# Kernel optimization log

Hardware: AMD Instinct MI355X
Metric: run time of the kernel (lower is better)

Reference implementation:

```python
import jax, jax.numpy as jnp
import numpy as np

N_NODES = 50000
NUM_FEATURES = 128
HIDDEN = 128
OUT = 64
N_EDGES = 600000


def gcn_conv(x, edge_index, W, b, n_nodes):
    """PyG GCNConv: add self-loops, symmetric deg^{-1/2} normalization,
    x' = D^{-1/2}(A+I)D^{-1/2} (x @ W) + b."""
    xw = x @ W  # [N, out]
    loop = jnp.arange(n_nodes, dtype=edge_index.dtype)
    row = jnp.concatenate([edge_index[0], loop])  # source
    col = jnp.concatenate([edge_index[1], loop])  # target
    ones = jnp.ones(row.shape[0], dtype=xw.dtype)
    deg = jax.ops.segment_sum(ones, col, num_segments=n_nodes)  # in-degree incl. self-loop
    dis = jnp.where(deg > 0, jax.lax.rsqrt(deg), 0.0)
    norm = dis[row] * dis[col]  # [E+N]
    msg = xw[row] * norm[:, None]  # gather + scale
    agg = jax.ops.segment_sum(msg, col, num_segments=n_nodes)  # scatter-add
    return agg + b


def setup_inputs() -> dict:
    key = jax.random.key(0)
    ks = jax.random.split(key, 10)
    x = jax.random.normal(ks[0], (N_NODES, NUM_FEATURES), dtype=jnp.float32)
    edge_index = jax.random.randint(ks[1], (2, N_EDGES), 0, N_NODES, dtype=jnp.int64)
    s1 = 1.0 / np.sqrt(NUM_FEATURES)
    s2 = 1.0 / np.sqrt(HIDDEN)
    s3 = 1.0 / np.sqrt(OUT)
    # encoder GCN weights stored as [in, out]
    W_enc1 = jax.random.uniform(ks[2], (NUM_FEATURES, HIDDEN), jnp.float32, -s1, s1)
    b_enc1 = jnp.zeros((HIDDEN,), jnp.float32)
    W_enc2 = jax.random.uniform(ks[3], (HIDDEN, OUT), jnp.float32, -s2, s2)
    b_enc2 = jnp.zeros((OUT,), jnp.float32)
    # decoder Linear weights stored as [in, out]
    W_dec1 = jax.random.uniform(ks[4], (OUT, HIDDEN), jnp.float32, -s3, s3)
    b_dec1 = jax.random.uniform(ks[5], (HIDDEN,), jnp.float32, -s3, s3)
    W_dec2 = jax.random.uniform(ks[6], (HIDDEN, NUM_FEATURES), jnp.float32, -s2, s2)
    b_dec2 = jax.random.uniform(ks[7], (NUM_FEATURES,), jnp.float32, -s2, s2)
    return {"x": x, "edge_index": edge_index,
            "W_enc1": W_enc1, "b_enc1": b_enc1,
            "W_enc2": W_enc2, "b_enc2": b_enc2,
            "W_dec1": W_dec1, "b_dec1": b_dec1,
            "W_dec2": W_dec2, "b_dec2": b_dec2}


def reference(x, edge_index, W_enc1, b_enc1, W_enc2, b_enc2,
              W_dec1, b_dec1, W_dec2, b_dec2):
    n = x.shape[0]
    z = jax.nn.relu(gcn_conv(x, edge_index, W_enc1, b_enc1, n))
    z = jax.nn.relu(gcn_conv(z, edge_index, W_enc2, b_enc2, n))
    z = jax.nn.relu(z @ W_dec1 + b_dec1)
    x_hat = z @ W_dec2 + b_dec2
    return x_hat
```

## Files before the change

kernel.cpp:

```cpp
#include <hip/hip_runtime.h>
#include <hip/hip_bf16.h>


#define N_FEAT 128
#define HID    128
#define OUTD   64

typedef __hip_bfloat16 bf16;
typedef unsigned short u16;
typedef __attribute__((ext_vector_type(8))) short short8;
typedef __attribute__((ext_vector_type(4))) float f32x4;

__device__ __forceinline__ float bs2f(short s) {
    return __builtin_bit_cast(float, ((unsigned)(unsigned short)s) << 16);
}
__device__ __forceinline__ short f2bs(float f) {
    __hip_bfloat16 h = __float2bfloat16(f);
    return __builtin_bit_cast(short, h);
}


__global__ void k_prep(int* __restrict__ cnt, int n, int ZB,
                       const float* __restrict__ W1, const float* __restrict__ W2,
                       const float* __restrict__ Wd1, const float* __restrict__ Wd2,
                       bf16* __restrict__ W1t, bf16* __restrict__ W2t,
                       bf16* __restrict__ Wd1t, bf16* __restrict__ Wd2t) {
    int b = blockIdx.x;
    if (b < ZB) {
        int i4 = b * 256 + threadIdx.x;
        int n4 = n >> 2;
        if (i4 < n4) ((int4*)cnt)[i4] = make_int4(0, 0, 0, 0);
        if (i4 == 0) for (int i = n4 * 4; i < n; ++i) cnt[i] = 0;
        return;
    }
    int i = (b - ZB) * 256 + threadIdx.x;
    if (i < 16384) {
        int k = i >> 7, nn = i & 127;
        W1t[nn * 128 + k] = __float2bfloat16(W1[i]);
    } else if (i < 24576) {
        int j = i - 16384; int k = j >> 6, nn = j & 63;
        W2t[nn * 128 + k] = __float2bfloat16(W2[j]);
    } else if (i < 32768) {
        int j = i - 24576; int k = j >> 7, nn = j & 127;
        Wd1t[nn * 64 + k] = __float2bfloat16(Wd1[j]);
    } else if (i < 49152) {
        int j = i - 32768; int k = j >> 7, nn = j & 127;
        Wd2t[nn * 128 + k] = __float2bfloat16(Wd2[j]);
    }
}


__global__ void k_mega(const int* __restrict__ row, const int* __restrict__ col,
                       int E, int SL, int npg, int GB,
                       int* __restrict__ cnt, u16* __restrict__ slots, int n,
                       const float* __restrict__ x, const bf16* __restrict__ W1t,
                       bf16* __restrict__ xw1) {
    int b = blockIdx.x;
    if (b < GB) {
        if (b * 64 >= n) return;
        int t = threadIdx.x;
        int lane = t & 63, w = t >> 6;
        int quad = lane >> 4, l16 = lane & 15;
        int m0 = b * 64 + (w & 1) * 32;
        int nhw = (w >> 1) * 32;
        int kq = quad * 8;

        short8 zero8 = {0, 0, 0, 0, 0, 0, 0, 0};
        int mrow[2]; bool mok[2];
#pragma unroll
        for (int mi = 0; mi < 2; ++mi) {
            mrow[mi] = m0 + mi * 16 + l16;
            mok[mi] = mrow[mi] < n;
        }
        short8 af[2][4];
#pragma unroll
        for (int mi = 0; mi < 2; ++mi) {
#pragma unroll
            for (int kb = 0; kb < 4; ++kb) {
                if (!mok[mi]) { af[mi][kb] = zero8; continue; }
                const float* Af = x + (size_t)mrow[mi] * 128 + kb * 32 + kq;
                float4 a4 = *(const float4*)Af;
                float4 b4 = *(const float4*)(Af + 4);
                short8 r = {f2bs(a4.x), f2bs(a4.y), f2bs(a4.z), f2bs(a4.w),
                            f2bs(b4.x), f2bs(b4.y), f2bs(b4.z), f2bs(b4.w)};
                af[mi][kb] = r;
            }
        }
#pragma unroll
        for (int nc = 0; nc < 128; nc += 64) {
            int n0 = nc + nhw;
            f32x4 acc[2][2];
#pragma unroll
            for (int mi = 0; mi < 2; ++mi)
#pragma unroll
                for (int ni = 0; ni < 2; ++ni)
#pragma unroll
                    for (int r = 0; r < 4; ++r) acc[mi][ni][r] = 0.f;
#pragma unroll
            for (int kb = 0; kb < 4; ++kb) {
                short8 bfm[2];
#pragma unroll
                for (int ni = 0; ni < 2; ++ni) {
                    int nn = n0 + ni * 16 + l16;
                    bfm[ni] = *(const short8*)(W1t + (size_t)nn * 128 + kb * 32 + kq);
                }
#pragma unroll
                for (int mi = 0; mi < 2; ++mi)
#pragma unroll
                    for (int ni = 0; ni < 2; ++ni)
                        acc[mi][ni] = __builtin_amdgcn_mfma_f32_16x16x32_bf16(
                            af[mi][kb], bfm[ni], acc[mi][ni], 0, 0, 0);
            }
#pragma unroll
            for (int ni = 0; ni < 2; ++ni) {
                int nn = n0 + ni * 16 + l16;
#pragma unroll
                for (int mi = 0; mi < 2; ++mi)
#pragma unroll
                    for (int r = 0; r < 4; ++r) {
                        int m = m0 + mi * 16 + quad * 4 + r;
                        if (m < n)
                            ((short*)xw1)[(size_t)m * 128 + nn] = f2bs(acc[mi][ni][r]);
                    }
            }
        }
        return;
    }
    int bb = b - GB;
    int g = bb & 7;
    int s = bb >> 3;
    int lo = g * npg;
    int hi = lo + npg; if (hi > n) hi = n;
    int i4 = s * 256 + threadIdx.x;
    int E4 = E >> 2;
    if (i4 < E4) {
        int4 r4 = ((const int4*)row)[i4];
        int4 c4 = ((const int4*)col)[i4];
        int rr[4] = {r4.x, r4.y, r4.z, r4.w};
        int cc[4] = {c4.x, c4.y, c4.z, c4.w};
#pragma unroll
        for (int u = 0; u < 4; ++u) {
            int r = rr[u], c = cc[u];
            if (c >= lo && c < hi && (unsigned)r < (unsigned)n) {
                int pos = atomicAdd(&cnt[c], 1);
                if (pos < 64) slots[(size_t)c * 64 + pos] = (u16)r;
            }
        }
    }
    if (i4 == 0) {
        for (int e = E4 * 4; e < E; ++e) {
            int r = row[e], c = col[e];
            if (c >= lo && c < hi && (unsigned)r < (unsigned)n) {
                int pos = atomicAdd(&cnt[c], 1);
                if (pos < 64) slots[(size_t)c * 64 + pos] = (u16)r;
            }
        }
    }
}


__global__ void k_aggmm(const bf16* __restrict__ xw1, const int* __restrict__ cnt,
                        const u16* __restrict__ slots, const float* __restrict__ b1,
                        const bf16* __restrict__ W2t, bf16* __restrict__ xw2, int M) {
    __shared__ short h1s[64][136];
    __shared__ u16 sl_s[64][72];
    __shared__ float dn_s[64];
    __shared__ int cn_s[64];
    int t = threadIdx.x;
    int lane = t & 63, w = t >> 6;
    int blk = blockIdx.x;

    if (t < 64) {
        int nd = blk * 64 + t;
        int craw = (nd < M) ? cnt[nd] : -1;
        cn_s[t] = (nd < M) ? (min(craw, 64) + 1) : 0;
        dn_s[t] = (nd < M) ? rsqrtf((float)(craw + 1)) : 0.f;
    }
    {
        int node = t >> 3, chunk = t & 7;
        int nd = blk * 64 + node;
        int4 val = make_int4(0, 0, 0, 0);
        if (nd < M)
            val = ((const int4*)(slots + (size_t)nd * 64))[chunk];
        *(int4*)&sl_s[node][chunk * 8] = val;
    }
    __syncthreads();

    int sub = lane >> 4, li = lane & 15;
    float4 c0 = *(const float4*)(b1 + li * 8);
    float4 c1 = *(const float4*)(b1 + li * 8 + 4);
    float bbv[8] = {c0.x, c0.y, c0.z, c0.w, c1.x, c1.y, c1.z, c1.w};

#pragma unroll
    for (int rnd = 0; rnd < 2; ++rnd) {
        int nl = w * 8 + rnd * 4 + sub;
        int nd = blk * 64 + nl;
        int cn = cn_s[nl];
        float a[8] = {0.f, 0.f, 0.f, 0.f, 0.f, 0.f, 0.f, 0.f};
        for (int tt = 0; tt < cn; tt += 8) {
            bool va[8]; short8 v[8]; float dsv[8];
#pragma unroll
            for (int u = 0; u < 8; ++u) {
                int ti = tt + u;
                va[u] = ti < cn;
                int tc = va[u] ? ti : 0;
                int sI = (tc == cn - 1) ? nd : (int)sl_s[nl][tc];
                v[u] = *((const short8*)(xw1 + (size_t)sI * 128) + li);
                dsv[u] = rsqrtf((float)(cnt[sI] + 1));
            }
#pragma unroll
            for (int u = 0; u < 8; ++u)
                if (va[u]) {
#pragma unroll
                    for (int j = 0; j < 8; ++j) a[j] += dsv[u] * bs2f(v[u][j]);
                }
        }
        float dn = dn_s[nl];
        short8 o;
#pragma unroll
        for (int j = 0; j < 8; ++j) o[j] = f2bs(fmaxf(dn * a[j] + bbv[j], 0.f));
        *(short8*)&h1s[nl][li * 8] = o;
    }
    __syncthreads();

    int quad = lane >> 4, l16 = lane & 15;
    int mt = w & 3;
    int nh = w >> 2;
    int kq = quad * 8;

    short8 af[4];
#pragma unroll
    for (int kb = 0; kb < 4; ++kb)
        af[kb] = *(const short8*)&h1s[mt * 16 + l16][kb * 32 + kq];

    f32x4 acc[2];
#pragma unroll
    for (int ni = 0; ni < 2; ++ni)
#pragma unroll
        for (int r = 0; r < 4; ++r) acc[ni][r] = 0.f;
#pragma unroll
    for (int kb = 0; kb < 4; ++kb) {
        short8 bfm[2];
#pragma unroll
        for (int ni = 0; ni < 2; ++ni) {
            int nn = nh * 32 + ni * 16 + l16;
            bfm[ni] = *(const short8*)(W2t + (size_t)nn * 128 + kb * 32 + kq);
        }
#pragma unroll
        for (int ni = 0; ni < 2; ++ni)
            acc[ni] = __builtin_amdgcn_mfma_f32_16x16x32_bf16(
                af[kb], bfm[ni], acc[ni], 0, 0, 0);
    }
#pragma unroll
    for (int ni = 0; ni < 2; ++ni) {
        int nn = nh * 32 + ni * 16 + l16;
#pragma unroll
        for (int r = 0; r < 4; ++r) {
            int ml = mt * 16 + quad * 4 + r;
            int m = blk * 64 + ml;
            if (m < M)
                ((short*)xw2)[(size_t)m * 64 + nn] = f2bs(acc[ni][r] * dn_s[ml]);
        }
    }
}


__global__ void k_aggdec(const bf16* __restrict__ xw2, const int* __restrict__ cnt,
                         const u16* __restrict__ slots,
                         const float* __restrict__ b2,
                         const bf16* __restrict__ Wd1t, const float* __restrict__ bd1,
                         const bf16* __restrict__ Wd2t, const float* __restrict__ bd2,
                         float* __restrict__ out, int M) {
    __shared__ short h2s[64][72];
    __shared__ short h3s[64][136];
    int t = threadIdx.x;
    int lane = t & 63, w = t >> 6;
    int quad = lane >> 4, l16 = lane & 15;
    int blk = blockIdx.x;

    {
        int sub = lane >> 3;
        int li = lane & 7;
        int sgl = w * 8 + sub;
        int nd0 = blk * 64 + sgl;
        int nd1 = nd0 + 32;
        int cr0 = (nd0 < M) ? cnt[nd0] : -1;
        int cr1 = (nd1 < M) ? cnt[nd1] : -1;
        int cn0 = (nd0 < M) ? min(cr0, 64) + 1 : 0;
        int cn1 = (nd1 < M) ? min(cr1, 64) + 1 : 0;
        const u16* sl0 = slots + (size_t)min(nd0, M - 1) * 64;
        const u16* sl1 = slots + (size_t)min(nd1, M - 1) * 64;

        float a0[8] = {0.f, 0.f, 0.f, 0.f, 0.f, 0.f, 0.f, 0.f};
        float a1[8] = {0.f, 0.f, 0.f, 0.f, 0.f, 0.f, 0.f, 0.f};
        int tmax = cn0 > cn1 ? cn0 : cn1;
        for (int e = 0; e < tmax; e += 4) {
            bool va0[4], va1[4]; short8 v0[4], v1[4];
#pragma unroll
            for (int u = 0; u < 4; ++u) {
                int ei_ = e + u;
                va0[u] = ei_ < cn0;
                int t0 = va0[u] ? ei_ : 0;
                int s0 = (t0 == cn0 - 1) ? nd0 : (int)sl0[t0];
                v0[u] = *((const short8*)(xw2 + (size_t)s0 * 64) + li);
                va1[u] = ei_ < cn1;
                int t1 = va1[u] ? ei_ : 0;
                int s1 = (t1 == cn1 - 1) ? nd1 : (int)sl1[t1];
                v1[u] = *((const short8*)(xw2 + (size_t)s1 * 64) + li);
            }
#pragma unroll
            for (int u = 0; u < 4; ++u) {
                if (va0[u]) {
#pragma unroll
                    for (int j = 0; j < 8; ++j) a0[j] += bs2f(v0[u][j]);
                }
                if (va1[u]) {
#pragma unroll
                    for (int j = 0; j < 8; ++j) a1[j] += bs2f(v1[u][j]);
                }
            }
        }
        float dn0 = (nd0 < M) ? rsqrtf((float)(cr0 + 1)) : 0.f;
        float dn1 = (nd1 < M) ? rsqrtf((float)(cr1 + 1)) : 0.f;
        float4 c0 = *(const float4*)(b2 + li * 8);
        float4 c1 = *(const float4*)(b2 + li * 8 + 4);
        float bb[8] = {c0.x, c0.y, c0.z, c0.w, c1.x, c1.y, c1.z, c1.w};
        short8 o0, o1;
#pragma unroll
        for (int j = 0; j < 8; ++j) {
            o0[j] = f2bs(fmaxf(dn0 * a0[j] + bb[j], 0.f));
            o1[j] = f2bs(fmaxf(dn1 * a1[j] + bb[j], 0.f));
        }
        *(short8*)&h2s[sgl][li * 8] = o0;
        *(short8*)&h2s[sgl + 32][li * 8] = o1;
    }
    __syncthreads();

    int m0 = (w & 1) * 32;
    int nhw = (w >> 1) * 32;
    int kq = quad * 8;

    short8 af1[2][2];
#pragma unroll
    for (int mi = 0; mi < 2; ++mi)
#pragma unroll
        for (int kb = 0; kb < 2; ++kb)
            af1[mi][kb] = *(const short8*)&h2s[m0 + mi * 16 + l16][kb * 32 + kq];

#pragma unroll
    for (int nc = 0; nc < HID; nc += 64) {
        int n0 = nc + nhw;
        f32x4 acc[2][2];
#pragma unroll
        for (int mi = 0; mi < 2; ++mi)
#pragma unroll
            for (int ni = 0; ni < 2; ++ni)
#pragma unroll
                for (int r = 0; r < 4; ++r) acc[mi][ni][r] = 0.f;
#pragma unroll
        for (int kb = 0; kb < 2; ++kb) {
            short8 bfm[2];
#pragma unroll
            for (int ni = 0; ni < 2; ++ni) {
                int nn = n0 + ni * 16 + l16;
                bfm[ni] = *(const short8*)(Wd1t + (size_t)nn * OUTD + kb * 32 + kq);
            }
#pragma unroll
            for (int mi = 0; mi < 2; ++mi)
#pragma unroll
                for (int ni = 0; ni < 2; ++ni)
                    acc[mi][ni] = __builtin_amdgcn_mfma_f32_16x16x32_bf16(
                        af1[mi][kb], bfm[ni], acc[mi][ni], 0, 0, 0);
        }
#pragma unroll
        for (int ni = 0; ni < 2; ++ni) {
            int nn = n0 + ni * 16 + l16;
            float bv = bd1[nn];
#pragma unroll
            for (int mi = 0; mi < 2; ++mi)
#pragma unroll
                for (int r = 0; r < 4; ++r) {
                    int ml = m0 + mi * 16 + quad * 4 + r;
                    h3s[ml][nn] = f2bs(fmaxf(acc[mi][ni][r] + bv, 0.f));
                }
        }
    }
    __syncthreads();

    short8 af2[2][4];
#pragma unroll
    for (int mi = 0; mi < 2; ++mi)
#pragma unroll
        for (int kb = 0; kb < 4; ++kb)
            af2[mi][kb] = *(const short8*)&h3s[m0 + mi * 16 + l16][kb * 32 + kq];

#pragma unroll
    for (int nc = 0; nc < N_FEAT; nc += 64) {
        int n0 = nc + nhw;
        f32x4 acc[2][2];
#pragma unroll
        for (int mi = 0; mi < 2; ++mi)
#pragma unroll
            for (int ni = 0; ni < 2; ++ni)
#pragma unroll
                for (int r = 0; r < 4; ++r) acc[mi][ni][r] = 0.f;
#pragma unroll
        for (int kb = 0; kb < 4; ++kb) {
            short8 bfm[2];
#pragma unroll
            for (int ni = 0; ni < 2; ++ni) {
                int nn = n0 + ni * 16 + l16;
                bfm[ni] = *(const short8*)(Wd2t + (size_t)nn * HID + kb * 32 + kq);
            }
#pragma unroll
            for (int mi = 0; mi < 2; ++mi)
#pragma unroll
                for (int ni = 0; ni < 2; ++ni)
                    acc[mi][ni] = __builtin_amdgcn_mfma_f32_16x16x32_bf16(
                        af2[mi][kb], bfm[ni], acc[mi][ni], 0, 0, 0);
        }
#pragma unroll
        for (int ni = 0; ni < 2; ++ni) {
            int nn = n0 + ni * 16 + l16;
            float bv = bd2[nn];
#pragma unroll
            for (int mi = 0; mi < 2; ++mi)
#pragma unroll
                for (int r = 0; r < 4; ++r) {
                    int m = blk * 64 + m0 + mi * 16 + quad * 4 + r;
                    if (m < M)
                        out[(size_t)m * N_FEAT + nn] = acc[mi][ni][r] + bv;
                }
        }
    }
}


extern "C" void kernel_launch(void* const* d_in, const int* in_sizes, int n_in,
                              void* d_out, int out_size, void* d_ws, size_t ws_size,
                              hipStream_t stream) {
    const float* x   = (const float*)d_in[0];
    const int*   ei  = (const int*)d_in[1];
    const float* W1  = (const float*)d_in[2];
    const float* b1  = (const float*)d_in[3];
    const float* W2  = (const float*)d_in[4];
    const float* b2  = (const float*)d_in[5];
    const float* Wd1 = (const float*)d_in[6];
    const float* bd1 = (const float*)d_in[7];
    const float* Wd2 = (const float*)d_in[8];
    const float* bd2 = (const float*)d_in[9];

    const int n = in_sizes[0] / N_FEAT;
    const int E = in_sizes[1] / 2;
    const int* row = ei;
    const int* col = ei + E;

    char* wp = (char*)d_ws;
    bf16* xw1 = (bf16*)wp;  wp += (size_t)n * 128 * 2;
    bf16* xw2 = (bf16*)wp;  wp += (size_t)n * 64 * 2;
    bf16* W1t = (bf16*)wp;  wp += 128 * 128 * 2;
    bf16* W2t = (bf16*)wp;  wp += 128 * 64 * 2;
    bf16* Wd1t= (bf16*)wp;  wp += 64 * 128 * 2;
    bf16* Wd2t= (bf16*)wp;  wp += 128 * 128 * 2;
    int* cnt   = (int*)wp;   wp += (size_t)n * 4;
    u16* slots = (u16*)wp;   wp += (size_t)n * 64 * 2;

    int ZB = (n + 1023) / 1024;
    k_prep<<<ZB + 192, 256, 0, stream>>>(cnt, n, ZB, W1, W2, Wd1, Wd2,
                                         W1t, W2t, Wd1t, Wd2t);

    int E4 = E >> 2;
    int SL = (E4 + 255) / 256;
    int npg = (n + 7) / 8;
    int mg = (n + 63) / 64;
    int GB = (mg + 7) & ~7;
    k_mega<<<GB + 8 * SL, 256, 0, stream>>>(row, col, E, SL, npg, GB,
                                            cnt, slots, n, x, W1t, xw1);

    k_aggmm<<<mg, 512, 0, stream>>>(xw1, cnt, slots, b1, W2t, xw2, n);

    k_aggdec<<<mg, 256, 0, stream>>>(xw2, cnt, slots, b2,
                                     Wd1t, bd1, Wd2t, bd2, (float*)d_out, n);
}
```

Measured before the change: 190.9 us.

## Restructure aggregate-decode kernel to 512 threads with LDS-staged slot lists

The final aggregation+decoder kernel now launches 512 threads per block, giving one 8-lane group per node instead of two nodes per group. Per-node neighbor slot lists and degree normalizers are staged into shared memory cooperatively before the gather. The gather unroll is raised to 8. The MFMA decoder stages are re-tiled so each of the 8 waves handles a 16-row by 64-column tile. The aim is more memory-level parallelism in the gather and less load imbalance from pairing nodes of different degrees. In exchange it uses more LDS and more registers per block, which could lower occupancy.

```diff
diff --git a/kernel.cpp b/kernel.cpp
--- a/kernel.cpp
+++ b/kernel.cpp
@@ -273,164 +273,138 @@
                          float* __restrict__ out, int M) {
     __shared__ short h2s[64][72];
     __shared__ short h3s[64][136];
+    __shared__ u16 sl_s[64][72];
+    __shared__ float dn_s[64];
+    __shared__ int cn_s[64];
     int t = threadIdx.x;
     int lane = t & 63, w = t >> 6;
-    int quad = lane >> 4, l16 = lane & 15;
     int blk = blockIdx.x;
 
+    if (t < 64) {
+        int nd = blk * 64 + t;
+        int craw = (nd < M) ? cnt[nd] : -1;
+        cn_s[t] = (nd < M) ? (min(craw, 64) + 1) : 0;
+        dn_s[t] = (nd < M) ? rsqrtf((float)(craw + 1)) : 0.f;
+    }
     {
-        int sub = lane >> 3;
-        int li = lane & 7;
-        int sgl = w * 8 + sub;
-        int nd0 = blk * 64 + sgl;
-        int nd1 = nd0 + 32;
-        int cr0 = (nd0 < M) ? cnt[nd0] : -1;
-        int cr1 = (nd1 < M) ? cnt[nd1] : -1;
-        int cn0 = (nd0 < M) ? min(cr0, 64) + 1 : 0;
-        int cn1 = (nd1 < M) ? min(cr1, 64) + 1 : 0;
-        const u16* sl0 = slots + (size_t)min(nd0, M - 1) * 64;
-        const u16* sl1 = slots + (size_t)min(nd1, M - 1) * 64;
-
-        float a0[8] = {0.f, 0.f, 0.f, 0.f, 0.f, 0.f, 0.f, 0.f};
-        float a1[8] = {0.f, 0.f, 0.f, 0.f, 0.f, 0.f, 0.f, 0.f};
-        int tmax = cn0 > cn1 ? cn0 : cn1;
-        for (int e = 0; e < tmax; e += 4) {
-            bool va0[4], va1[4]; short8 v0[4], v1[4];
-#pragma unroll
-            for (int u = 0; u < 4; ++u) {
-                int ei_ = e + u;
-                va0[u] = ei_ < cn0;
-                int t0 = va0[u] ? ei_ : 0;
-                int s0 = (t0 == cn0 - 1) ? nd0 : (int)sl0[t0];
-                v0[u] = *((const short8*)(xw2 + (size_t)s0 * 64) + li);
-                va1[u] = ei_ < cn1;
-                int t1 = va1[u] ? ei_ : 0;
-                int s1 = (t1 == cn1 - 1) ? nd1 : (int)sl1[t1];
-                v1[u] = *((const short8*)(xw2 + (size_t)s1 * 64) + li);
-            }
-#pragma unroll
-            for (int u = 0; u < 4; ++u) {
-                if (va0[u]) {
-#pragma unroll
-                    for (int j = 0; j < 8; ++j) a0[j] += bs2f(v0[u][j]);
+        int node = t >> 3, chunk = t & 7;
+        int nd = blk * 64 + node;
+        int4 val = make_int4(0, 0, 0, 0);
+        if (nd < M)
+            val = ((const int4*)(slots + (size_t)nd * 64))[chunk];
+        *(int4*)&sl_s[node][chunk * 8] = val;
+    }
+    __syncthreads();
+
+    {
+        int grp = t >> 3, li = t & 7;
+        int nd = blk * 64 + grp;
+        int cn = cn_s[grp];
+        float a[8] = {0.f, 0.f, 0.f, 0.f, 0.f, 0.f, 0.f, 0.f};
+        for (int tt = 0; tt < cn; tt += 8) {
+            bool va[8]; short8 v[8];
+#pragma unroll
+            for (int u = 0; u < 8; ++u) {
+                int ti = tt + u;
+                va[u] = ti < cn;
+                int tc = va[u] ? ti : 0;
+                int sI = (tc == cn - 1) ? nd : (int)sl_s[grp][tc];
+                v[u] = *((const short8*)(xw2 + (size_t)sI * 64) + li);
+            }
+#pragma unroll
+            for (int u = 0; u < 8; ++u)
+                if (va[u]) {
+#pragma unroll
+                    for (int j = 0; j < 8; ++j) a[j] += bs2f(v[u][j]);
                 }
-                if (va1[u]) {
-#pragma unroll
-                    for (int j = 0; j < 8; ++j) a1[j] += bs2f(v1[u][j]);
-                }
-            }
-        }
-        float dn0 = (nd0 < M) ? rsqrtf((float)(cr0 + 1)) : 0.f;
-        float dn1 = (nd1 < M) ? rsqrtf((float)(cr1 + 1)) : 0.f;
+        }
+        float dn = dn_s[grp];
         float4 c0 = *(const float4*)(b2 + li * 8);
         float4 c1 = *(const float4*)(b2 + li * 8 + 4);
         float bb[8] = {c0.x, c0.y, c0.z, c0.w, c1.x, c1.y, c1.z, c1.w};
-        short8 o0, o1;
-#pragma unroll
-        for (int j = 0; j < 8; ++j) {
-            o0[j] = f2bs(fmaxf(dn0 * a0[j] + bb[j], 0.f));
-            o1[j] = f2bs(fmaxf(dn1 * a1[j] + bb[j], 0.f));
-        }
-        *(short8*)&h2s[sgl][li * 8] = o0;
-        *(short8*)&h2s[sgl + 32][li * 8] = o1;
+        short8 o;
+#pragma unroll
+        for (int j = 0; j < 8; ++j) o[j] = f2bs(fmaxf(dn * a[j] + bb[j], 0.f));
+        *(short8*)&h2s[grp][li * 8] = o;
     }
     __syncthreads();
 
-    int m0 = (w & 1) * 32;
-    int nhw = (w >> 1) * 32;
+    int quad = lane >> 4, l16 = lane & 15;
+    int mt = w & 3;
+    int nh = w >> 2;
     int kq = quad * 8;
 
-    short8 af1[2][2];
-#pragma unroll
-    for (int mi = 0; mi < 2; ++mi)
+    {
+        short8 af1[2];
 #pragma unroll
         for (int kb = 0; kb < 2; ++kb)
-            af1[mi][kb] = *(const short8*)&h2s[m0 + mi * 16 + l16][kb * 32 + kq];
-
-#pragma unroll
-    for (int nc = 0; nc < HID; nc += 64) {
-        int n0 = nc + nhw;
-        f32x4 acc[2][2];
-#pragma unroll
-        for (int mi = 0; mi < 2; ++mi)
-#pragma unroll
-            for (int ni = 0; ni < 2; ++ni)
-#pragma unroll
-                for (int r = 0; r < 4; ++r) acc[mi][ni][r] = 0.f;
+            af1[kb] = *(const short8*)&h2s[mt * 16 + l16][kb * 32 + kq];
+
+        f32x4 acc[4];
+#pragma unroll
+        for (int ni = 0; ni < 4; ++ni)
+#pragma unroll
+            for (int r = 0; r < 4; ++r) acc[ni][r] = 0.f;
 #pragma unroll
         for (int kb = 0; kb < 2; ++kb) {
-            short8 bfm[2];
-#pragma unroll
-            for (int ni = 0; ni < 2; ++ni) {
-                int nn = n0 + ni * 16 + l16;
+            short8 bfm[4];
+#pragma unroll
+            for (int ni = 0; ni < 4; ++ni) {
+                int nn = nh * 64 + ni * 16 + l16;
                 bfm[ni] = *(const short8*)(Wd1t + (size_t)nn * OUTD + kb * 32 + kq);
             }
 #pragma unroll
-            for (int mi = 0; mi < 2; ++mi)
-#pragma unroll
-                for (int ni = 0; ni < 2; ++ni)
-                    acc[mi][ni] = __builtin_amdgcn_mfma_f32_16x16x32_bf16(
-                        af1[mi][kb], bfm[ni], acc[mi][ni], 0, 0, 0);
-        }
-#pragma unroll
-        for (int ni = 0; ni < 2; ++ni) {
-            int nn = n0 + ni * 16 + l16;
+            for (int ni = 0; ni < 4; ++ni)
+                acc[ni] = __builtin_amdgcn_mfma_f32_16x16x32_bf16(
+                    af1[kb], bfm[ni], acc[ni], 0, 0, 0);
+        }
+#pragma unroll
+        for (int ni = 0; ni < 4; ++ni) {
+            int nn = nh * 64 + ni * 16 + l16;
             float bv = bd1[nn];
 #pragma unroll
-            for (int mi = 0; mi < 2; ++mi)
-#pragma unroll
-                for (int r = 0; r < 4; ++r) {
-                    int ml = m0 + mi * 16 + quad * 4 + r;
-                    h3s[ml][nn] = f2bs(fmaxf(acc[mi][ni][r] + bv, 0.f));
-                }
+            for (int r = 0; r < 4; ++r) {
+                int ml = mt * 16 + quad * 4 + r;
+                h3s[ml][nn] = f2bs(fmaxf(acc[ni][r] + bv, 0.f));
+            }
         }
     }
     __syncthreads();
 
-    short8 af2[2][4];
-#pragma unroll
-    for (int mi = 0; mi < 2; ++mi)
+    {
+        short8 af2[4];
 #pragma unroll
         for (int kb = 0; kb < 4; ++kb)
-            af2[mi][kb] = *(const short8*)&h3s[m0 + mi * 16 + l16][kb * 32 + kq];
-
-#pragma unroll
-    for (int nc = 0; nc < N_FEAT; nc += 64) {
-        int n0 = nc + nhw;
-        f32x4 acc[2][2];
-#pragma unroll
-        for (int mi = 0; mi < 2; ++mi)
-#pragma unroll
-            for (int ni = 0; ni < 2; ++ni)
-#pragma unroll
-                for (int r = 0; r < 4; ++r) acc[mi][ni][r] = 0.f;
+            af2[kb] = *(const short8*)&h3s[mt * 16 + l16][kb * 32 + kq];
+
+        f32x4 acc[4];
+#pragma unroll
+        for (int ni = 0; ni < 4; ++ni)
+#pragma unroll
+            for (int r = 0; r < 4; ++r) acc[ni][r] = 0.f;
 #pragma unroll
         for (int kb = 0; kb < 4; ++kb) {
-            short8 bfm[2];
-#pragma unroll
-            for (int ni = 0; ni < 2; ++ni) {
-                int nn = n0 + ni * 16 + l16;
+            short8 bfm[4];
+#pragma unroll
+            for (int ni = 0; ni < 4; ++ni) {
+                int nn = nh * 64 + ni * 16 + l16;
                 bfm[ni] = *(const short8*)(Wd2t + (size_t)nn * HID + kb * 32 + kq);
             }
 #pragma unroll
-            for (int mi = 0; mi < 2; ++mi)
-#pragma unroll
-                for (int ni = 0; ni < 2; ++ni)
-                    acc[mi][ni] = __builtin_amdgcn_mfma_f32_16x16x32_bf16(
-                        af2[mi][kb], bfm[ni], acc[mi][ni], 0, 0, 0);
-        }
-#pragma unroll
-        for (int ni = 0; ni < 2; ++ni) {
-            int nn = n0 + ni * 16 + l16;
+            for (int ni = 0; ni < 4; ++ni)
+                acc[ni] = __builtin_amdgcn_mfma_f32_16x16x32_bf16(
+                    af2[kb], bfm[ni], acc[ni], 0, 0, 0);
+        }
+#pragma unroll
+        for (int ni = 0; ni < 4; ++ni) {
+            int nn = nh * 64 + ni * 16 + l16;
             float bv = bd2[nn];
 #pragma unroll
-            for (int mi = 0; mi < 2; ++mi)
-#pragma unroll
-                for (int r = 0; r < 4; ++r) {
-                    int m = blk * 64 + m0 + mi * 16 + quad * 4 + r;
-                    if (m < M)
-                        out[(size_t)m * N_FEAT + nn] = acc[mi][ni][r] + bv;
-                }
+            for (int r = 0; r < 4; ++r) {
+                int m = blk * 64 + mt * 16 + quad * 4 + r;
+                if (m < M)
+                    out[(size_t)m * N_FEAT + nn] = acc[ni][r] + bv;
+            }
         }
     }
 }
@@ -479,6 +453,6 @@
 
     k_aggmm<<<mg, 512, 0, stream>>>(xw1, cnt, slots, b1, W2t, xw2, n);
 
-    k_aggdec<<<mg, 256, 0, stream>>>(xw2, cnt, slots, b2,
+    k_aggdec<<<mg, 512, 0, stream>>>(xw2, cnt, slots, b2,
                                      Wd1t, bd1, Wd2t, bd2, (float*)d_out, n);
 }
```

Result: no change. 193.0 us (median of 2 runs) (+1.1%).
